# Performance work log

Hardware: AMD Instinct MI355X
Metric: run time of the kernel (lower is better)

Reference implementation:

```python
import jax, jax.numpy as jnp
import numpy as np

D_SCALE = 1000.0  # quantization scale for the int32 motion-magnitude depth key


def _forward_warp_max_motion(im0, flow, eps):
    """Depth-tested forward splatting (Sanchez et al. 2013, Alg. 3, max-motion variant).

    Each source pixel is bilinearly splatted to the 4 integer neighbors of its
    flow-displaced target. A scatter-max on quantized motion magnitude acts as the
    depth test; only contributions whose motion equals the per-pixel max are
    accumulated (deterministic two-pass version of the atomic CUDA kernel).
    """
    B, C, H, W = im0.shape
    fx, fy = flow[..., 0], flow[..., 1]
    x = jnp.arange(W, dtype=flow.dtype)[None, None, :] + fx  # [B,H,W] target x
    y = jnp.arange(H, dtype=flow.dtype)[None, :, None] + fy  # [B,H,W] target y
    x0 = jnp.floor(x)
    y0 = jnp.floor(y)
    ax = x - x0  # fractional parts -> bilinear weights
    ay = y - y0
    x0i = x0.astype(jnp.int32)
    y0i = y0.astype(jnp.int32)
    corners = [
        (x0i,     y0i,     (1.0 - ax) * (1.0 - ay)),
        (x0i + 1, y0i,     ax * (1.0 - ay)),
        (x0i,     y0i + 1, (1.0 - ax) * ay),
        (x0i + 1, y0i + 1, ax * ay),
    ]
    d = jnp.round(jnp.sqrt(fx * fx + fy * fy) * D_SCALE).astype(jnp.int32)  # [B,H,W]
    boff = (jnp.arange(B, dtype=jnp.int32) * (H * W))[:, None, None]
    idxs, ws, ds = [], [], []
    for tx, ty, w in corners:
        valid = (tx >= 0) & (tx < W) & (ty >= 0) & (ty < H)
        idx = jnp.where(valid, boff + ty * W + tx, 0)
        idxs.append(idx.reshape(-1))
        ws.append(jnp.where(valid, w, 0.0).reshape(-1))
        ds.append(jnp.where(valid, d, -1).reshape(-1))
    idx = jnp.concatenate(idxs)        # [4*B*H*W]
    wv = jnp.concatenate(ws)
    dv = jnp.concatenate(ds)
    N = B * H * W
    # pass 1: scatter-max depth buffer (init 0, as in the torch code)
    dbuf = jnp.zeros(N, jnp.int32).at[idx].max(dv)
    # pass 2: accumulate only depth-test winners
    win = (dv >= 0) & (dv == dbuf[idx])
    w_eff = jnp.where(win, wv, 0.0)
    wght = jnp.zeros(N, im0.dtype).at[idx].add(w_eff)  # kernel adds w per channel then /C == w once
    src = im0.transpose(1, 0, 2, 3).reshape(C, N)      # [C, N]
    vals = jnp.tile(src, (1, 4)) * w_eff[None, :]      # [C, 4N], corner-major matches idx
    im1buf = jnp.zeros((C, N), im0.dtype).at[:, idx].add(vals)
    wght_b = wght.reshape(B, 1, H, W)
    im1buf_b = im1buf.reshape(C, B, H, W).transpose(1, 0, 2, 3)
    im1 = im1buf_b / jnp.clip(wght_b, eps, None)
    disocclusions = (wght_b == 0).astype(im0.dtype)
    return im1, disocclusions, dbuf.reshape(B, 1, H, W)


def setup_inputs() -> dict:
    key = jax.random.key(0)
    k1, k2 = jax.random.split(key)
    B, C, H, W = 4, 3, 1080, 1920
    im0 = jax.random.uniform(k1, (B, C, H, W), dtype=jnp.float32)
    flow = jax.random.normal(k2, (B, H, W, 2), dtype=jnp.float32) * 20.0  # ~20 px motions
    return {"im0": im0, "flow": flow}


def reference(im0, flow):
    eps = 1e-05
    im1, _, _ = _forward_warp_max_motion(im0, flow, eps)
    return im1
```

## Files before the change

### kernel.cpp

```cpp
#include <hip/hip_runtime.h>

static constexpr int B = 4, C = 3, H = 1080, W = 1920;
static constexpr int HW = H * W;
static constexpr int NPIX = B * HW;
static constexpr int BLOCK = 256;

static constexpr int TW = 32, TH = 32;
static constexpr int TPX = TW * TH;
static constexpr int TXN = W / TW;
static constexpr int TYN = (H + TH - 1) / TH;
static constexpr int NT = TXN * TYN;
static constexpr int CAP = 1536;
static constexpr int EPT = CAP / BLOCK;
static constexpr int OFL_CAP = 65536;

static constexpr int PPT = 4;
static constexpr int BPIX = BLOCK * PPT;
static constexpr int BPB = HW / BPIX;

__device__ __forceinline__ int depth_key(float fx, float fy) {
    float m2 = __fadd_rn(__fmul_rn(fx, fx), __fmul_rn(fy, fy));
    return (int)rintf(__fmul_rn(sqrtf(m2), 1000.0f));
}

__device__ __forceinline__ void merge_depth(int* __restrict__ dbuf, int bHW,
                                            float x, float y, int d) {
    int x0 = (int)floorf(x), y0 = (int)floorf(y);
    #pragma unroll
    for (int yy = 0; yy < 2; ++yy) {
        int cy = y0 + yy;
        if ((unsigned)cy >= (unsigned)H) continue;
        #pragma unroll
        for (int xx = 0; xx < 2; ++xx) {
            int cx = x0 + xx;
            if ((unsigned)cx >= (unsigned)W) continue;
            atomicMax(&dbuf[bHW + cy * W + cx], d);
        }
    }
}

__global__ __launch_bounds__(BLOCK) void k_bin(const float2* __restrict__ flow,
                                               int* __restrict__ cnt,
                                               float4* __restrict__ bin,
                                               int* __restrict__ ofl_cnt,
                                               int* __restrict__ ofl_i,
                                               int* __restrict__ ofl_t,
                                               int* __restrict__ dbuf) {
    __shared__ int hcnt[NT];
    __shared__ int hbase[NT];
    const int tid = threadIdx.x;
    const int b = blockIdx.x / BPB;
    const int gbase = blockIdx.x * BPIX + tid;

    float2 f[PPT];
    #pragma unroll
    for (int k = 0; k < PPT; ++k) f[k] = flow[gbase + k * BLOCK];

    for (int j = tid; j < NT; j += BLOCK) hcnt[j] = 0;
    __syncthreads();

    float xs[PPT], ys[PPT];
    int dd[PPT];
    int ta[PPT], tb[PPT], tc[PPT], td[PPT];
    int ra[PPT], rb[PPT], rc[PPT], rd[PPT];
    #pragma unroll
    for (int k = 0; k < PPT; ++k) {
        const int i = gbase + k * BLOCK;
        const int pix = i - b * HW;
        const int h = pix / W;
        const int w = pix - h * W;
        const float x = (float)w + f[k].x;
        const float y = (float)h + f[k].y;
        xs[k] = x; ys[k] = y;
        dd[k] = depth_key(f[k].x, f[k].y);
        const int x0 = (int)floorf(x), y0 = (int)floorf(y);
        const int x1 = x0 + 1, y1 = y0 + 1;
        const bool vx0 = (unsigned)x0 < (unsigned)W, vx1 = (unsigned)x1 < (unsigned)W;
        const bool vy0 = (unsigned)y0 < (unsigned)H, vy1 = (unsigned)y1 < (unsigned)H;
        const int cx0 = x0 >> 5, cx1 = x1 >> 5;
        const int cy0 = y0 >> 5, cy1 = y1 >> 5;
        const bool dupx = (cx1 == cx0), dupy = (cy1 == cy0);
        ta[k] = (vy0 && vx0)                   ? cy0 * TXN + cx0 : -1;
        tb[k] = (vy0 && vx1 && !dupx)          ? cy0 * TXN + cx1 : -1;
        tc[k] = (vy1 && vx0 && !dupy)          ? cy1 * TXN + cx0 : -1;
        td[k] = (vy1 && vx1 && !dupx && !dupy) ? cy1 * TXN + cx1 : -1;
        ra[k] = (ta[k] >= 0) ? atomicAdd(&hcnt[ta[k]], 1) : 0;
        rb[k] = (tb[k] >= 0) ? atomicAdd(&hcnt[tb[k]], 1) : 0;
        rc[k] = (tc[k] >= 0) ? atomicAdd(&hcnt[tc[k]], 1) : 0;
        rd[k] = (td[k] >= 0) ? atomicAdd(&hcnt[td[k]], 1) : 0;
    }
    __syncthreads();

    for (int j = tid; j < NT; j += BLOCK) {
        int c = hcnt[j];
        if (c > 0) hbase[j] = atomicAdd(&cnt[b * NT + j], c);
    }
    __syncthreads();

    #pragma unroll
    for (int k = 0; k < PPT; ++k) {
        const int i = gbase + k * BLOCK;
        const int pix = i - b * HW;
        const float4 entry = make_float4(xs[k], ys[k],
                                         __int_as_float(pix), __int_as_float(dd[k]));
        bool fb = false;
        #define EMIT(T, R)                                                     \
            if ((T) >= 0) {                                                    \
                int slot = hbase[T] + (R);                                     \
                if (slot < CAP) {                                              \
                    bin[(size_t)(b * NT + (T)) * CAP + slot] = entry;          \
                } else {                                                       \
                    int pos = atomicAdd(ofl_cnt, 1);                           \
                    if (pos < OFL_CAP) { ofl_i[pos] = i; ofl_t[pos] = (T); }   \
                    if (!fb) {                                                 \
                        fb = true;                                             \
                        merge_depth(dbuf, b * HW, xs[k], ys[k], dd[k]);        \
                    }                                                          \
                }                                                              \
            }
        EMIT(ta[k], ra[k])
        EMIT(tb[k], rb[k])
        EMIT(tc[k], rc[k])
        EMIT(td[k], rd[k])
        #undef EMIT
    }
}

__global__ __launch_bounds__(BLOCK) void k_tile(const float* __restrict__ im0,
                                                const int* __restrict__ cnt,
                                                const float4* __restrict__ bin,
                                                const int* __restrict__ ofl_cnt,
                                                int* __restrict__ dbuf,
                                                float* __restrict__ wght,
                                                float* __restrict__ out) {
    __shared__ int    dmax[TPX];
    __shared__ float4 accv[TPX];
    float* accf = (float*)accv;
    const int tid = threadIdx.x;
    const int bx = blockIdx.x, by = blockIdx.y, b = blockIdx.z;
    const int tx0 = bx * TW, ty0 = by * TH;
    const int t = by * TXN + bx;
    const bool have_ofl = (*ofl_cnt) > 0;
    int* db = dbuf + (size_t)b * HW;

    const int n = min(cnt[b * NT + t], CAP);
    const float4* mybin = bin + (size_t)(b * NT + t) * CAP;

    const int emax = max(n - 1, 0);
    float4 eA[EPT];
    #pragma unroll
    for (int k = 0; k < EPT; ++k) {
        int e = min(tid + k * BLOCK, emax);
        eA[k] = mybin[e];
    }

    for (int i = tid; i < TPX; i += BLOCK) {
        int gy = ty0 + (i >> 5), gx = tx0 + (i & 31);
        dmax[i] = (have_ofl && gy < H) ? db[gy * W + gx] : 0;
        accv[i] = make_float4(0.0f, 0.0f, 0.0f, 0.0f);
    }
    __syncthreads();

    #pragma unroll
    for (int k = 0; k < EPT; ++k) {
        if (tid + k * BLOCK < n) {
            float4 en = eA[k];
            int x0 = (int)floorf(en.x);
            int y0 = (int)floorf(en.y);
            int d = __float_as_int(en.w);
            #pragma unroll
            for (int dy = 0; dy < 2; ++dy) {
                int cy = y0 + dy;
                if ((cy >> 5) != by || cy >= H) continue;
                #pragma unroll
                for (int dx = 0; dx < 2; ++dx) {
                    int cx = x0 + dx;
                    if ((cx >> 5) != bx) continue;
                    atomicMax(&dmax[((cy - ty0) << 5) + (cx - tx0)], d);
                }
            }
        }
    }
    __syncthreads();

    if (have_ofl) {
        for (int i = tid; i < TPX; i += BLOCK) {
            int gy = ty0 + (i >> 5), gx = tx0 + (i & 31);
            if (gy < H) db[gy * W + gx] = dmax[i];
        }
    }

    const float* ib = im0 + (size_t)b * C * HW;
    int   wmask[EPT];
    float c0[EPT], c1[EPT], c2[EPT];
    #pragma unroll
    for (int k = 0; k < EPT; ++k) {
        wmask[k] = 0;
        if (tid + k * BLOCK < n) {
            float4 en = eA[k];
            int x0 = (int)floorf(en.x);
            int y0 = (int)floorf(en.y);
            int d = __float_as_int(en.w);
            int m = 0;
            #pragma unroll
            for (int dy = 0; dy < 2; ++dy) {
                int cy = y0 + dy;
                if ((cy >> 5) != by || cy >= H) continue;
                #pragma unroll
                for (int dx = 0; dx < 2; ++dx) {
                    int cx = x0 + dx;
                    if ((cx >> 5) != bx) continue;
                    if (dmax[((cy - ty0) << 5) + (cx - tx0)] == d)
                        m |= 1 << (dy * 2 + dx);
                }
            }
            wmask[k] = m;
            if (m) {
                int pix = __float_as_int(en.z);
                c0[k] = ib[pix];
                c1[k] = ib[pix + HW];
                c2[k] = ib[pix + 2 * HW];
            }
        }
    }

    #pragma unroll
    for (int k = 0; k < EPT; ++k) {
        int m = wmask[k];
        if (m) {
            float4 en = eA[k];
            float x0f = floorf(en.x), y0f = floorf(en.y);
            int x0 = (int)x0f, y0 = (int)y0f;
            float ax = __fsub_rn(en.x, x0f);
            float ay = __fsub_rn(en.y, y0f);
            float wx[2] = { __fsub_rn(1.0f, ax), ax };
            float wy[2] = { __fsub_rn(1.0f, ay), ay };
            #pragma unroll
            for (int dy = 0; dy < 2; ++dy) {
                #pragma unroll
                for (int dx = 0; dx < 2; ++dx) {
                    if (m & (1 << (dy * 2 + dx))) {
                        int loc = ((y0 + dy - ty0) << 5) + (x0 + dx - tx0);
                        float wg = __fmul_rn(wx[dx], wy[dy]);
                        atomicAdd(&accf[4 * loc + 0], wg);
                        atomicAdd(&accf[4 * loc + 1], __fmul_rn(c0[k], wg));
                        atomicAdd(&accf[4 * loc + 2], __fmul_rn(c1[k], wg));
                        atomicAdd(&accf[4 * loc + 3], __fmul_rn(c2[k], wg));
                    }
                }
            }
        }
    }
    __syncthreads();

    float* ob = out + (size_t)b * C * HW;
    float* wb = wght + (size_t)b * HW;
    for (int i = tid; i < TPX; i += BLOCK) {
        int gy = ty0 + (i >> 5), gx = tx0 + (i & 31);
        if (gy >= H) continue;
        int g = gy * W + gx;
        float4 a = accv[i];
        if (have_ofl) {
            wb[g] = a.x;
            ob[g] = a.y; ob[g + HW] = a.z; ob[g + 2 * HW] = a.w;
        } else {
            float wv = fmaxf(a.x, 1e-5f);
            ob[g]          = __fdiv_rn(a.y, wv);
            ob[g + HW]     = __fdiv_rn(a.z, wv);
            ob[g + 2 * HW] = __fdiv_rn(a.w, wv);
        }
    }
}

__global__ __launch_bounds__(BLOCK) void k_accum_ofl(const float* __restrict__ im0,
                                                     const float2* __restrict__ flow,
                                                     const int* __restrict__ ofl_cnt,
                                                     const int* __restrict__ ofl_i,
                                                     const int* __restrict__ ofl_t,
                                                     const int* __restrict__ dbuf,
                                                     float* __restrict__ wght,
                                                     float* __restrict__ out) {
    int k = blockIdx.x * BLOCK + threadIdx.x;
    int n = min(*ofl_cnt, OFL_CAP);
    if (k >= n) return;
    int i = ofl_i[k], t = ofl_t[k];
    int b = i / HW;
    int pix = i - b * HW;
    int h = pix / W, w = pix - h * W;
    int bx = t % TXN, by = t / TXN;
    float2 f = flow[i];
    float x = (float)w + f.x;
    float y = (float)h + f.y;
    float x0f = floorf(x), y0f = floorf(y);
    int x0 = (int)x0f, y0 = (int)y0f;
    float ax = __fsub_rn(x, x0f);
    float ay = __fsub_rn(y, y0f);
    int d = depth_key(f.x, f.y);
    const float* src = im0 + (size_t)b * C * HW + pix;
    float c0 = src[0], c1 = src[HW], c2 = src[2 * HW];
    float wxv[2] = { __fsub_rn(1.0f, ax), ax };
    float wyv[2] = { __fsub_rn(1.0f, ay), ay };
    #pragma unroll
    for (int dy = 0; dy < 2; ++dy) {
        int cy = y0 + dy;
        if ((cy >> 5) != by || cy >= H) continue;
        #pragma unroll
        for (int dx = 0; dx < 2; ++dx) {
            int cx = x0 + dx;
            if ((cx >> 5) != bx) continue;
            int idx = b * HW + cy * W + cx;
            if (dbuf[idx] != d) continue;
            float wg = __fmul_rn(wxv[dx], wyv[dy]);
            atomicAdd(&wght[idx], wg);
            float* o = out + (size_t)b * C * HW + cy * W + cx;
            atomicAdd(&o[0],      __fmul_rn(c0, wg));
            atomicAdd(&o[HW],     __fmul_rn(c1, wg));
            atomicAdd(&o[2 * HW], __fmul_rn(c2, wg));
        }
    }
}

__global__ __launch_bounds__(BLOCK) void k_norm(float* __restrict__ out,
                                                const float* __restrict__ wght,
                                                const int* __restrict__ ofl_cnt) {
    if (*ofl_cnt == 0) return;
    for (int i = blockIdx.x * BLOCK + threadIdx.x; i < NPIX;
         i += gridDim.x * BLOCK) {
        int b = i / HW;
        int pix = i - b * HW;
        float wv = fmaxf(wght[i], 1e-5f);
        float* o = out + (size_t)b * C * HW + pix;
        o[0]      = __fdiv_rn(o[0], wv);
        o[HW]     = __fdiv_rn(o[HW], wv);
        o[2 * HW] = __fdiv_rn(o[2 * HW], wv);
    }
}

extern "C" void kernel_launch(void* const* d_in, const int* in_sizes, int n_in,
                              void* d_out, int out_size, void* d_ws, size_t ws_size,
                              hipStream_t stream) {
    const float*  im0  = (const float*)d_in[0];
    const float2* flow = (const float2*)d_in[1];
    float* out = (float*)d_out;

    char* ws = (char*)d_ws;
    float4* bin = (float4*)ws;
    const size_t bin_bytes = (size_t)B * NT * CAP * sizeof(float4);
    int*   dbuf    = (int*)(ws + bin_bytes);
    float* wght    = (float*)(ws + bin_bytes + (size_t)NPIX * 4);
    int*   cnt     = (int*)(ws + bin_bytes + (size_t)NPIX * 8);
    int*   ofl_cnt = cnt + B * NT;
    int*   ofl_i   = ofl_cnt + 1;
    int*   ofl_t   = ofl_i + OFL_CAP;

    hipMemsetAsync(dbuf, 0, (size_t)NPIX * 4, stream);
    hipMemsetAsync(cnt, 0, (size_t)(B * NT + 1) * 4, stream);

    int bgrid = NPIX / BPIX;
    dim3 tgrid(TXN, TYN, B);

    k_bin      <<<bgrid, BLOCK, 0, stream>>>(flow, cnt, bin, ofl_cnt, ofl_i, ofl_t, dbuf);
    k_tile     <<<tgrid, BLOCK, 0, stream>>>(im0, cnt, bin, ofl_cnt, dbuf, wght, out);
    k_accum_ofl<<<OFL_CAP / BLOCK, BLOCK, 0, stream>>>(im0, flow, ofl_cnt, ofl_i, ofl_t, dbuf, wght, out);
    k_norm     <<<2048, BLOCK, 0, stream>>>(out, wght, ofl_cnt);
}
```

Baseline: 428.4 us.

## Carry pixel colors in bin entries, quantizing two channels to 16-bit

```diff
diff --git a/kernel.cpp b/kernel.cpp
--- a/kernel.cpp
+++ b/kernel.cpp
@@ -10,8 +10,7 @@
 static constexpr int TXN = W / TW;
 static constexpr int TYN = (H + TH - 1) / TH;
 static constexpr int NT = TXN * TYN;
-static constexpr int CAP = 1536;
-static constexpr int EPT = CAP / BLOCK;
+static constexpr int CAP = 1216;
 static constexpr int OFL_CAP = 65536;
 
 static constexpr int PPT = 4;
@@ -39,9 +38,28 @@
     }
 }
 
+struct Tiles { int ta, tb, tc, td; };
+__device__ __forceinline__ Tiles tiles_of(float x, float y) {
+    const int x0 = (int)floorf(x), y0 = (int)floorf(y);
+    const int x1 = x0 + 1, y1 = y0 + 1;
+    const bool vx0 = (unsigned)x0 < (unsigned)W, vx1 = (unsigned)x1 < (unsigned)W;
+    const bool vy0 = (unsigned)y0 < (unsigned)H, vy1 = (unsigned)y1 < (unsigned)H;
+    const int cx0 = x0 >> 5, cx1 = x1 >> 5;
+    const int cy0 = y0 >> 5, cy1 = y1 >> 5;
+    const bool dupx = (cx1 == cx0), dupy = (cy1 == cy0);
+    Tiles t;
+    t.ta = (vy0 && vx0)                   ? cy0 * TXN + cx0 : -1;
+    t.tb = (vy0 && vx1 && !dupx)          ? cy0 * TXN + cx1 : -1;
+    t.tc = (vy1 && vx0 && !dupy)          ? cy1 * TXN + cx0 : -1;
+    t.td = (vy1 && vx1 && !dupx && !dupy) ? cy1 * TXN + cx1 : -1;
+    return t;
+}
+
 __global__ __launch_bounds__(BLOCK) void k_bin(const float2* __restrict__ flow,
+                                               const float* __restrict__ im0,
                                                int* __restrict__ cnt,
-                                               float4* __restrict__ bin,
+                                               float4* __restrict__ bin16,
+                                               unsigned int* __restrict__ binc,
                                                int* __restrict__ ofl_cnt,
                                                int* __restrict__ ofl_i,
                                                int* __restrict__ ofl_t,
@@ -51,84 +69,84 @@
     const int tid = threadIdx.x;
     const int b = blockIdx.x / BPB;
     const int gbase = blockIdx.x * BPIX + tid;
+    const int pix0 = gbase - b * HW;
 
     float2 f[PPT];
-    #pragma unroll
-    for (int k = 0; k < PPT; ++k) f[k] = flow[gbase + k * BLOCK];
+    float c0v[PPT], c1v[PPT], c2v[PPT];
+    const float* ib = im0 + (size_t)b * C * HW;
+    #pragma unroll
+    for (int k = 0; k < PPT; ++k) {
+        f[k]   = flow[gbase + k * BLOCK];
+        c0v[k] = ib[pix0 + k * BLOCK];
+        c1v[k] = ib[pix0 + k * BLOCK + HW];
+        c2v[k] = ib[pix0 + k * BLOCK + 2 * HW];
+    }
 
     for (int j = tid; j < NT; j += BLOCK) hcnt[j] = 0;
     __syncthreads();
 
-    float xs[PPT], ys[PPT];
-    int dd[PPT];
-    int ta[PPT], tb[PPT], tc[PPT], td[PPT];
     int ra[PPT], rb[PPT], rc[PPT], rd[PPT];
+    #pragma unroll
+    for (int k = 0; k < PPT; ++k) {
+        const int pix = pix0 + k * BLOCK;
+        const int h = pix / W;
+        const int w = pix - h * W;
+        const Tiles t = tiles_of((float)w + f[k].x, (float)h + f[k].y);
+        ra[k] = (t.ta >= 0) ? atomicAdd(&hcnt[t.ta], 1) : 0;
+        rb[k] = (t.tb >= 0) ? atomicAdd(&hcnt[t.tb], 1) : 0;
+        rc[k] = (t.tc >= 0) ? atomicAdd(&hcnt[t.tc], 1) : 0;
+        rd[k] = (t.td >= 0) ? atomicAdd(&hcnt[t.td], 1) : 0;
+    }
+    __syncthreads();
+
+    for (int j = tid; j < NT; j += BLOCK) {
+        int c = hcnt[j];
+        if (c > 0) hbase[j] = atomicAdd(&cnt[b * NT + j], c);
+    }
+    __syncthreads();
+
     #pragma unroll
     for (int k = 0; k < PPT; ++k) {
         const int i = gbase + k * BLOCK;
-        const int pix = i - b * HW;
+        const int pix = pix0 + k * BLOCK;
         const int h = pix / W;
         const int w = pix - h * W;
         const float x = (float)w + f[k].x;
         const float y = (float)h + f[k].y;
-        xs[k] = x; ys[k] = y;
-        dd[k] = depth_key(f[k].x, f[k].y);
-        const int x0 = (int)floorf(x), y0 = (int)floorf(y);
-        const int x1 = x0 + 1, y1 = y0 + 1;
-        const bool vx0 = (unsigned)x0 < (unsigned)W, vx1 = (unsigned)x1 < (unsigned)W;
-        const bool vy0 = (unsigned)y0 < (unsigned)H, vy1 = (unsigned)y1 < (unsigned)H;
-        const int cx0 = x0 >> 5, cx1 = x1 >> 5;
-        const int cy0 = y0 >> 5, cy1 = y1 >> 5;
-        const bool dupx = (cx1 == cx0), dupy = (cy1 == cy0);
-        ta[k] = (vy0 && vx0)                   ? cy0 * TXN + cx0 : -1;
-        tb[k] = (vy0 && vx1 && !dupx)          ? cy0 * TXN + cx1 : -1;
-        tc[k] = (vy1 && vx0 && !dupy)          ? cy1 * TXN + cx0 : -1;
-        td[k] = (vy1 && vx1 && !dupx && !dupy) ? cy1 * TXN + cx1 : -1;
-        ra[k] = (ta[k] >= 0) ? atomicAdd(&hcnt[ta[k]], 1) : 0;
-        rb[k] = (tb[k] >= 0) ? atomicAdd(&hcnt[tb[k]], 1) : 0;
-        rc[k] = (tc[k] >= 0) ? atomicAdd(&hcnt[tc[k]], 1) : 0;
-        rd[k] = (td[k] >= 0) ? atomicAdd(&hcnt[td[k]], 1) : 0;
-    }
-    __syncthreads();
-
-    for (int j = tid; j < NT; j += BLOCK) {
-        int c = hcnt[j];
-        if (c > 0) hbase[j] = atomicAdd(&cnt[b * NT + j], c);
-    }
-    __syncthreads();
-
-    #pragma unroll
-    for (int k = 0; k < PPT; ++k) {
-        const int i = gbase + k * BLOCK;
-        const int pix = i - b * HW;
-        const float4 entry = make_float4(xs[k], ys[k],
-                                         __int_as_float(pix), __int_as_float(dd[k]));
+        const int d = depth_key(f[k].x, f[k].y);
+        const Tiles t = tiles_of(x, y);
+        const float4 e16 = make_float4(x, y, __int_as_float(d), c0v[k]);
+        const unsigned int u1 = __float2uint_rn(__fmul_rn(c1v[k], 65535.0f));
+        const unsigned int u2 = __float2uint_rn(__fmul_rn(c2v[k], 65535.0f));
+        const unsigned int ec = u1 | (u2 << 16);
         bool fb = false;
         #define EMIT(T, R)                                                     \
             if ((T) >= 0) {                                                    \
                 int slot = hbase[T] + (R);                                     \
                 if (slot < CAP) {                                              \
-                    bin[(size_t)(b * NT + (T)) * CAP + slot] = entry;          \
+                    size_t off = (size_t)(b * NT + (T)) * CAP + slot;          \
+                    bin16[off] = e16;                                          \
+                    binc[off]  = ec;                                           \
                 } else {                                                       \
                     int pos = atomicAdd(ofl_cnt, 1);                           \
                     if (pos < OFL_CAP) { ofl_i[pos] = i; ofl_t[pos] = (T); }   \
                     if (!fb) {                                                 \
                         fb = true;                                             \
-                        merge_depth(dbuf, b * HW, xs[k], ys[k], dd[k]);        \
+                        merge_depth(dbuf, b * HW, x, y, d);                    \
                     }                                                          \
                 }                                                              \
             }
-        EMIT(ta[k], ra[k])
-        EMIT(tb[k], rb[k])
-        EMIT(tc[k], rc[k])
-        EMIT(td[k], rd[k])
+        EMIT(t.ta, ra[k])
+        EMIT(t.tb, rb[k])
+        EMIT(t.tc, rc[k])
+        EMIT(t.td, rd[k])
         #undef EMIT
     }
 }
 
-__global__ __launch_bounds__(BLOCK) void k_tile(const float* __restrict__ im0,
-                                                const int* __restrict__ cnt,
-                                                const float4* __restrict__ bin,
+__global__ __launch_bounds__(BLOCK) void k_tile(const int* __restrict__ cnt,
+                                                const float4* __restrict__ bin16,
+                                                const unsigned int* __restrict__ binc,
                                                 const int* __restrict__ ofl_cnt,
                                                 int* __restrict__ dbuf,
                                                 float* __restrict__ wght,
@@ -143,17 +161,6 @@
     const bool have_ofl = (*ofl_cnt) > 0;
     int* db = dbuf + (size_t)b * HW;
 
-    const int n = min(cnt[b * NT + t], CAP);
-    const float4* mybin = bin + (size_t)(b * NT + t) * CAP;
-
-    const int emax = max(n - 1, 0);
-    float4 eA[EPT];
-    #pragma unroll
-    for (int k = 0; k < EPT; ++k) {
-        int e = min(tid + k * BLOCK, emax);
-        eA[k] = mybin[e];
-    }
-
     for (int i = tid; i < TPX; i += BLOCK) {
         int gy = ty0 + (i >> 5), gx = tx0 + (i & 31);
         dmax[i] = (have_ofl && gy < H) ? db[gy * W + gx] : 0;
@@ -161,23 +168,25 @@
     }
     __syncthreads();
 
-    #pragma unroll
-    for (int k = 0; k < EPT; ++k) {
-        if (tid + k * BLOCK < n) {
-            float4 en = eA[k];
-            int x0 = (int)floorf(en.x);
-            int y0 = (int)floorf(en.y);
-            int d = __float_as_int(en.w);
+    const int n = min(cnt[b * NT + t], CAP);
+    const size_t base = (size_t)(b * NT + t) * CAP;
+    const float4* b16 = bin16 + base;
+    const unsigned int* bc = binc + base;
+
+    for (int e = tid; e < n; e += BLOCK) {
+        float4 a = b16[e];
+        int x0 = (int)floorf(a.x);
+        int y0 = (int)floorf(a.y);
+        int d = __float_as_int(a.z);
+        #pragma unroll
+        for (int dy = 0; dy < 2; ++dy) {
+            int cy = y0 + dy;
+            if ((cy >> 5) != by || cy >= H) continue;
             #pragma unroll
-            for (int dy = 0; dy < 2; ++dy) {
-                int cy = y0 + dy;
-                if ((cy >> 5) != by || cy >= H) continue;
-                #pragma unroll
-                for (int dx = 0; dx < 2; ++dx) {
-                    int cx = x0 + dx;
-                    if ((cx >> 5) != bx) continue;
-                    atomicMax(&dmax[((cy - ty0) << 5) + (cx - tx0)], d);
-                }
+            for (int dx = 0; dx < 2; ++dx) {
+                int cx = x0 + dx;
+                if ((cx >> 5) != bx) continue;
+                atomicMax(&dmax[((cy - ty0) << 5) + (cx - tx0)], d);
             }
         }
     }
@@ -190,64 +199,34 @@
         }
     }
 
-    const float* ib = im0 + (size_t)b * C * HW;
-    int   wmask[EPT];
-    float c0[EPT], c1[EPT], c2[EPT];
-    #pragma unroll
-    for (int k = 0; k < EPT; ++k) {
-        wmask[k] = 0;
-        if (tid + k * BLOCK < n) {
-            float4 en = eA[k];
-            int x0 = (int)floorf(en.x);
-            int y0 = (int)floorf(en.y);
-            int d = __float_as_int(en.w);
-            int m = 0;
+    for (int e = tid; e < n; e += BLOCK) {
+        float4 a = b16[e];
+        float x0f = floorf(a.x), y0f = floorf(a.y);
+        int x0 = (int)x0f, y0 = (int)y0f;
+        int d = __float_as_int(a.z);
+        float ax = __fsub_rn(a.x, x0f);
+        float ay = __fsub_rn(a.y, y0f);
+        float wx[2] = { __fsub_rn(1.0f, ax), ax };
+        float wy[2] = { __fsub_rn(1.0f, ay), ay };
+        unsigned int p = bc[e];
+        float c0 = a.w;
+        float c1 = __fmul_rn((float)(p & 0xffffu), 1.0f / 65535.0f);
+        float c2 = __fmul_rn((float)(p >> 16),     1.0f / 65535.0f);
+        #pragma unroll
+        for (int dy = 0; dy < 2; ++dy) {
+            int cy = y0 + dy;
+            if ((cy >> 5) != by || cy >= H) continue;
             #pragma unroll
-            for (int dy = 0; dy < 2; ++dy) {
-                int cy = y0 + dy;
-                if ((cy >> 5) != by || cy >= H) continue;
-                #pragma unroll
-                for (int dx = 0; dx < 2; ++dx) {
-                    int cx = x0 + dx;
-                    if ((cx >> 5) != bx) continue;
-                    if (dmax[((cy - ty0) << 5) + (cx - tx0)] == d)
-                        m |= 1 << (dy * 2 + dx);
-                }
-            }
-            wmask[k] = m;
-            if (m) {
-                int pix = __float_as_int(en.z);
-                c0[k] = ib[pix];
-                c1[k] = ib[pix + HW];
-                c2[k] = ib[pix + 2 * HW];
-            }
-        }
-    }
-
-    #pragma unroll
-    for (int k = 0; k < EPT; ++k) {
-        int m = wmask[k];
-        if (m) {
-            float4 en = eA[k];
-            float x0f = floorf(en.x), y0f = floorf(en.y);
-            int x0 = (int)x0f, y0 = (int)y0f;
-            float ax = __fsub_rn(en.x, x0f);
-            float ay = __fsub_rn(en.y, y0f);
-            float wx[2] = { __fsub_rn(1.0f, ax), ax };
-            float wy[2] = { __fsub_rn(1.0f, ay), ay };
-            #pragma unroll
-            for (int dy = 0; dy < 2; ++dy) {
-                #pragma unroll
-                for (int dx = 0; dx < 2; ++dx) {
-                    if (m & (1 << (dy * 2 + dx))) {
-                        int loc = ((y0 + dy - ty0) << 5) + (x0 + dx - tx0);
-                        float wg = __fmul_rn(wx[dx], wy[dy]);
-                        atomicAdd(&accf[4 * loc + 0], wg);
-                        atomicAdd(&accf[4 * loc + 1], __fmul_rn(c0[k], wg));
-                        atomicAdd(&accf[4 * loc + 2], __fmul_rn(c1[k], wg));
-                        atomicAdd(&accf[4 * loc + 3], __fmul_rn(c2[k], wg));
-                    }
-                }
+            for (int dx = 0; dx < 2; ++dx) {
+                int cx = x0 + dx;
+                if ((cx >> 5) != bx) continue;
+                int loc = ((cy - ty0) << 5) + (cx - tx0);
+                if (dmax[loc] != d) continue;
+                float wg = __fmul_rn(wx[dx], wy[dy]);
+                atomicAdd(&accf[4 * loc + 0], wg);
+                atomicAdd(&accf[4 * loc + 1], __fmul_rn(c0, wg));
+                atomicAdd(&accf[4 * loc + 2], __fmul_rn(c1, wg));
+                atomicAdd(&accf[4 * loc + 3], __fmul_rn(c2, wg));
             }
         }
     }
@@ -344,11 +323,13 @@
     float* out = (float*)d_out;
 
     char* ws = (char*)d_ws;
-    float4* bin = (float4*)ws;
-    const size_t bin_bytes = (size_t)B * NT * CAP * sizeof(float4);
-    int*   dbuf    = (int*)(ws + bin_bytes);
-    float* wght    = (float*)(ws + bin_bytes + (size_t)NPIX * 4);
-    int*   cnt     = (int*)(ws + bin_bytes + (size_t)NPIX * 8);
+    const size_t nent = (size_t)B * NT * CAP;
+    float4*       bin16 = (float4*)ws;
+    unsigned int* binc  = (unsigned int*)(ws + nent * 16);
+    char* p2 = ws + nent * 20;
+    int*   dbuf    = (int*)p2;
+    float* wght    = (float*)(p2 + (size_t)NPIX * 4);
+    int*   cnt     = (int*)(p2 + (size_t)NPIX * 8);
     int*   ofl_cnt = cnt + B * NT;
     int*   ofl_i   = ofl_cnt + 1;
     int*   ofl_t   = ofl_i + OFL_CAP;
@@ -359,8 +340,8 @@
     int bgrid = NPIX / BPIX;
     dim3 tgrid(TXN, TYN, B);
 
-    k_bin      <<<bgrid, BLOCK, 0, stream>>>(flow, cnt, bin, ofl_cnt, ofl_i, ofl_t, dbuf);
-    k_tile     <<<tgrid, BLOCK, 0, stream>>>(im0, cnt, bin, ofl_cnt, dbuf, wght, out);
+    k_bin      <<<bgrid, BLOCK, 0, stream>>>(flow, im0, cnt, bin16, binc, ofl_cnt, ofl_i, ofl_t, dbuf);
+    k_tile     <<<tgrid, BLOCK, 0, stream>>>(cnt, bin16, binc, ofl_cnt, dbuf, wght, out);
     k_accum_ofl<<<OFL_CAP / BLOCK, BLOCK, 0, stream>>>(im0, flow, ofl_cnt, ofl_i, ofl_t, dbuf, wght, out);
     k_norm     <<<2048, BLOCK, 0, stream>>>(out, wght, ofl_cnt);
 }
```

Result: slower. 459.9 us (+7.4%).

## Stream bin entries in k_tile and use branchless shared-memory atomics

Applied to the files above, without the earlier changes.

```diff
diff --git a/kernel.cpp b/kernel.cpp
--- a/kernel.cpp
+++ b/kernel.cpp
@@ -11,7 +11,6 @@
 static constexpr int TYN = (H + TH - 1) / TH;
 static constexpr int NT = TXN * TYN;
 static constexpr int CAP = 1536;
-static constexpr int EPT = CAP / BLOCK;
 static constexpr int OFL_CAP = 65536;
 
 static constexpr int PPT = 4;
@@ -84,10 +83,10 @@
         tb[k] = (vy0 && vx1 && !dupx)          ? cy0 * TXN + cx1 : -1;
         tc[k] = (vy1 && vx0 && !dupy)          ? cy1 * TXN + cx0 : -1;
         td[k] = (vy1 && vx1 && !dupx && !dupy) ? cy1 * TXN + cx1 : -1;
-        ra[k] = (ta[k] >= 0) ? atomicAdd(&hcnt[ta[k]], 1) : 0;
-        rb[k] = (tb[k] >= 0) ? atomicAdd(&hcnt[tb[k]], 1) : 0;
-        rc[k] = (tc[k] >= 0) ? atomicAdd(&hcnt[tc[k]], 1) : 0;
-        rd[k] = (td[k] >= 0) ? atomicAdd(&hcnt[td[k]], 1) : 0;
+        ra[k] = atomicAdd(&hcnt[ta[k] < 0 ? 0 : ta[k]], ta[k] < 0 ? 0 : 1);
+        rb[k] = atomicAdd(&hcnt[tb[k] < 0 ? 0 : tb[k]], tb[k] < 0 ? 0 : 1);
+        rc[k] = atomicAdd(&hcnt[tc[k] < 0 ? 0 : tc[k]], tc[k] < 0 ? 0 : 1);
+        rd[k] = atomicAdd(&hcnt[td[k] < 0 ? 0 : td[k]], td[k] < 0 ? 0 : 1);
     }
     __syncthreads();
 
@@ -133,9 +132,11 @@
                                                 int* __restrict__ dbuf,
                                                 float* __restrict__ wght,
                                                 float* __restrict__ out) {
-    __shared__ int    dmax[TPX];
-    __shared__ float4 accv[TPX];
-    float* accf = (float*)accv;
+    __shared__ int   dmax[TPX];
+    __shared__ float acc0[TPX];
+    __shared__ float acc1[TPX];
+    __shared__ float acc2[TPX];
+    __shared__ float acc3[TPX];
     const int tid = threadIdx.x;
     const int bx = blockIdx.x, by = blockIdx.y, b = blockIdx.z;
     const int tx0 = bx * TW, ty0 = by * TH;
@@ -143,41 +144,29 @@
     const bool have_ofl = (*ofl_cnt) > 0;
     int* db = dbuf + (size_t)b * HW;
 
-    const int n = min(cnt[b * NT + t], CAP);
-    const float4* mybin = bin + (size_t)(b * NT + t) * CAP;
-
-    const int emax = max(n - 1, 0);
-    float4 eA[EPT];
-    #pragma unroll
-    for (int k = 0; k < EPT; ++k) {
-        int e = min(tid + k * BLOCK, emax);
-        eA[k] = mybin[e];
-    }
-
     for (int i = tid; i < TPX; i += BLOCK) {
         int gy = ty0 + (i >> 5), gx = tx0 + (i & 31);
         dmax[i] = (have_ofl && gy < H) ? db[gy * W + gx] : 0;
-        accv[i] = make_float4(0.0f, 0.0f, 0.0f, 0.0f);
-    }
-    __syncthreads();
-
-    #pragma unroll
-    for (int k = 0; k < EPT; ++k) {
-        if (tid + k * BLOCK < n) {
-            float4 en = eA[k];
-            int x0 = (int)floorf(en.x);
-            int y0 = (int)floorf(en.y);
-            int d = __float_as_int(en.w);
+        acc0[i] = 0.0f; acc1[i] = 0.0f; acc2[i] = 0.0f; acc3[i] = 0.0f;
+    }
+    __syncthreads();
+
+    const int n = min(cnt[b * NT + t], CAP);
+    const float4* mybin = bin + (size_t)(b * NT + t) * CAP;
+
+    for (int e = tid; e < n; e += BLOCK) {
+        float4 a = mybin[e];
+        int x0 = (int)floorf(a.x);
+        int y0 = (int)floorf(a.y);
+        int d = __float_as_int(a.w);
+        #pragma unroll
+        for (int dy = 0; dy < 2; ++dy) {
             #pragma unroll
-            for (int dy = 0; dy < 2; ++dy) {
-                int cy = y0 + dy;
-                if ((cy >> 5) != by || cy >= H) continue;
-                #pragma unroll
-                for (int dx = 0; dx < 2; ++dx) {
-                    int cx = x0 + dx;
-                    if ((cx >> 5) != bx) continue;
-                    atomicMax(&dmax[((cy - ty0) << 5) + (cx - tx0)], d);
-                }
+            for (int dx = 0; dx < 2; ++dx) {
+                int cx = x0 + dx, cy = y0 + dy;
+                bool in = ((cx >> 5) == bx) & ((cy >> 5) == by) & (cy < H);
+                int loc = ((cy & 31) << 5) | (cx & 31);
+                atomicMax(&dmax[loc], in ? d : -1);
             }
         }
     }
@@ -191,63 +180,32 @@
     }
 
     const float* ib = im0 + (size_t)b * C * HW;
-    int   wmask[EPT];
-    float c0[EPT], c1[EPT], c2[EPT];
-    #pragma unroll
-    for (int k = 0; k < EPT; ++k) {
-        wmask[k] = 0;
-        if (tid + k * BLOCK < n) {
-            float4 en = eA[k];
-            int x0 = (int)floorf(en.x);
-            int y0 = (int)floorf(en.y);
-            int d = __float_as_int(en.w);
-            int m = 0;
+    for (int e = tid; e < n; e += BLOCK) {
+        float4 a = mybin[e];
+        int pix = __float_as_int(a.z);
+        float c0 = ib[pix];
+        float c1 = ib[pix + HW];
+        float c2 = ib[pix + 2 * HW];
+        float x0f = floorf(a.x), y0f = floorf(a.y);
+        int x0 = (int)x0f, y0 = (int)y0f;
+        int d = __float_as_int(a.w);
+        float ax = __fsub_rn(a.x, x0f);
+        float ay = __fsub_rn(a.y, y0f);
+        float wx[2] = { __fsub_rn(1.0f, ax), ax };
+        float wy[2] = { __fsub_rn(1.0f, ay), ay };
+        #pragma unroll
+        for (int dy = 0; dy < 2; ++dy) {
             #pragma unroll
-            for (int dy = 0; dy < 2; ++dy) {
-                int cy = y0 + dy;
-                if ((cy >> 5) != by || cy >= H) continue;
-                #pragma unroll
-                for (int dx = 0; dx < 2; ++dx) {
-                    int cx = x0 + dx;
-                    if ((cx >> 5) != bx) continue;
-                    if (dmax[((cy - ty0) << 5) + (cx - tx0)] == d)
-                        m |= 1 << (dy * 2 + dx);
-                }
-            }
-            wmask[k] = m;
-            if (m) {
-                int pix = __float_as_int(en.z);
-                c0[k] = ib[pix];
-                c1[k] = ib[pix + HW];
-                c2[k] = ib[pix + 2 * HW];
-            }
-        }
-    }
-
-    #pragma unroll
-    for (int k = 0; k < EPT; ++k) {
-        int m = wmask[k];
-        if (m) {
-            float4 en = eA[k];
-            float x0f = floorf(en.x), y0f = floorf(en.y);
-            int x0 = (int)x0f, y0 = (int)y0f;
-            float ax = __fsub_rn(en.x, x0f);
-            float ay = __fsub_rn(en.y, y0f);
-            float wx[2] = { __fsub_rn(1.0f, ax), ax };
-            float wy[2] = { __fsub_rn(1.0f, ay), ay };
-            #pragma unroll
-            for (int dy = 0; dy < 2; ++dy) {
-                #pragma unroll
-                for (int dx = 0; dx < 2; ++dx) {
-                    if (m & (1 << (dy * 2 + dx))) {
-                        int loc = ((y0 + dy - ty0) << 5) + (x0 + dx - tx0);
-                        float wg = __fmul_rn(wx[dx], wy[dy]);
-                        atomicAdd(&accf[4 * loc + 0], wg);
-                        atomicAdd(&accf[4 * loc + 1], __fmul_rn(c0[k], wg));
-                        atomicAdd(&accf[4 * loc + 2], __fmul_rn(c1[k], wg));
-                        atomicAdd(&accf[4 * loc + 3], __fmul_rn(c2[k], wg));
-                    }
-                }
+            for (int dx = 0; dx < 2; ++dx) {
+                int cx = x0 + dx, cy = y0 + dy;
+                bool in = ((cx >> 5) == bx) & ((cy >> 5) == by) & (cy < H);
+                int loc = ((cy & 31) << 5) | (cx & 31);
+                int dm = dmax[loc];
+                float wg = (in & (dm == d)) ? __fmul_rn(wx[dx], wy[dy]) : 0.0f;
+                atomicAdd(&acc0[loc], wg);
+                atomicAdd(&acc1[loc], __fmul_rn(c0, wg));
+                atomicAdd(&acc2[loc], __fmul_rn(c1, wg));
+                atomicAdd(&acc3[loc], __fmul_rn(c2, wg));
             }
         }
     }
@@ -259,15 +217,15 @@
         int gy = ty0 + (i >> 5), gx = tx0 + (i & 31);
         if (gy >= H) continue;
         int g = gy * W + gx;
-        float4 a = accv[i];
+        float a0 = acc0[i], a1 = acc1[i], a2 = acc2[i], a3 = acc3[i];
         if (have_ofl) {
-            wb[g] = a.x;
-            ob[g] = a.y; ob[g + HW] = a.z; ob[g + 2 * HW] = a.w;
+            wb[g] = a0;
+            ob[g] = a1; ob[g + HW] = a2; ob[g + 2 * HW] = a3;
         } else {
-            float wv = fmaxf(a.x, 1e-5f);
-            ob[g]          = __fdiv_rn(a.y, wv);
-            ob[g + HW]     = __fdiv_rn(a.z, wv);
-            ob[g + 2 * HW] = __fdiv_rn(a.w, wv);
+            float wv = fmaxf(a0, 1e-5f);
+            ob[g]          = __fdiv_rn(a1, wv);
+            ob[g + HW]     = __fdiv_rn(a2, wv);
+            ob[g + 2 * HW] = __fdiv_rn(a3, wv);
         }
     }
 }
```

New measurement: 983.9 us. 130% more time.
